# Kernel tuning notes

Measured on AMD Instinct MI355X. Metric: run time of the kernel, lower is better.

## Reference

```python
import jax, jax.numpy as jnp
import numpy as np


def setup_inputs() -> dict:
    key = jax.random.key(0)
    k1, k2 = jax.random.split(key)
    x = jax.random.normal(k1, (64, 64, 64, 64), dtype=jnp.float32)
    embeddings = jax.random.normal(k2, (400, 64), dtype=jnp.float32) * 0.1
    return {"x": x, "embeddings": embeddings}


def reference(x, embeddings):
    D = embeddings.shape[1]
    flat_x = x.reshape(-1, D)  # [N, D]
    # squared L2 distance via sum-of-squares + matmul: [N, K]
    distances = (
        jnp.sum(flat_x * flat_x, axis=1, keepdims=True)
        + jnp.sum(embeddings * embeddings, axis=1)
        - 2.0 * jnp.matmul(flat_x, embeddings.T)
    )
    encoding_indices = jnp.argmin(distances, axis=1)  # [N]
    quantized = jnp.take(embeddings, encoding_indices, axis=0)  # [N, D]
    return quantized.reshape(x.shape)
```

## Files before the change

### kernel.cpp

```cpp
#include <hip/hip_runtime.h>

#define D 64
#define K 400
#define KT 25
#define BLOCK 256
#define WPB (BLOCK / 64)
#define NRM_OFF 102400

typedef _Float16 f16x8 __attribute__((ext_vector_type(8)));
typedef float f32x4 __attribute__((ext_vector_type(4)));
typedef int i32x4 __attribute__((ext_vector_type(4)));


__global__ void vq_prep(const float* __restrict__ emb, void* __restrict__ ws) {
  _Float16* B = (_Float16*)ws;
  float* nrm = (float*)((char*)ws + NRM_OFF);
  int gid = blockIdx.x * blockDim.x + threadIdx.x;
  if (gid < KT * 4 * 64) {
    int t = gid >> 8;
    int f = (gid >> 6) & 3;
    int l = gid & 63;
    int code = t * 16 + (l & 15);
    int kb = ((l >> 4) << 3) + ((f >> 1) << 5);
    const float* ep = emb + code * D + kb;
    float4 u = *(const float4*)ep;
    float4 w = *(const float4*)(ep + 4);
    f16x8 h;
    if ((f & 1) == 0) {
      h[0] = (_Float16)(2.0f * u.x);
      h[1] = (_Float16)(2.0f * u.y);
      h[2] = (_Float16)(2.0f * u.z);
      h[3] = (_Float16)(2.0f * u.w);
      h[4] = (_Float16)(2.0f * w.x);
      h[5] = (_Float16)(2.0f * w.y);
      h[6] = (_Float16)(2.0f * w.z);
      h[7] = (_Float16)(2.0f * w.w);
    } else {
#define LOC(j, val)                                    \
      do {                                             \
        float s_ = 2.0f * (val);                       \
        _Float16 t_ = (_Float16)s_;                    \
        h[j] = (_Float16)((s_ - (float)t_) * 2048.0f); \
      } while (0)
      LOC(0, u.x); LOC(1, u.y); LOC(2, u.z); LOC(3, u.w);
      LOC(4, w.x); LOC(5, w.y); LOC(6, w.z); LOC(7, w.w);
#undef LOC
    }
    *(f16x8*)&B[gid * 8] = h;
  }
  if (gid < K) {
    const float4* ep = (const float4*)(emb + (size_t)gid * D);
    float4 s4 = {0.f, 0.f, 0.f, 0.f};
#pragma unroll
    for (int d = 0; d < 16; ++d) {
      float4 v = ep[d];
      s4.x = fmaf(v.x, v.x, s4.x);
      s4.y = fmaf(v.y, v.y, s4.y);
      s4.z = fmaf(v.z, v.z, s4.z);
      s4.w = fmaf(v.w, v.w, s4.w);
    }
    nrm[gid] = (s4.x + s4.y) + (s4.z + s4.w);
  }
}

#define SPL(hh, ll, j, val)                          \
  do {                                               \
    float v_ = (val);                                \
    _Float16 t_ = (_Float16)v_;                      \
    (hh)[j] = t_;                                    \
    (ll)[j] = (_Float16)((v_ - (float)t_) * 2048.0f);\
  } while (0)

__global__ __launch_bounds__(BLOCK) void vq_mfma(
    const float* __restrict__ x,
    const float* __restrict__ emb,
    const void* __restrict__ ws,
    float* __restrict__ out,
    int nrows) {
  const f16x8* B = (const f16x8*)ws;
  const float* nrm = (const float*)((const char*)ws + NRM_OFF);

  const int tid = threadIdx.x;
  const int lane = tid & 63;
  const int wid = tid >> 6;
  const int gw = blockIdx.x * WPB + wid;
  const int nw = gridDim.x * WPB;
  const int l15 = lane & 15;
  const int q = lane >> 4;

#define LOADX(a)                                                   \
  do {                                                             \
    const float* xp_ = x + (size_t)(row0 + (a)*16 + l15) * D + q * 8; \
    float4 u0_ = *(const float4*)xp_;                              \
    float4 u1_ = *(const float4*)(xp_ + 4);                        \
    float4 w0_ = *(const float4*)(xp_ + 32);                       \
    float4 w1_ = *(const float4*)(xp_ + 36);                       \
    SPL(xh##a##0, xl##a##0, 0, u0_.x);                             \
    SPL(xh##a##0, xl##a##0, 1, u0_.y);                             \
    SPL(xh##a##0, xl##a##0, 2, u0_.z);                             \
    SPL(xh##a##0, xl##a##0, 3, u0_.w);                             \
    SPL(xh##a##0, xl##a##0, 4, u1_.x);                             \
    SPL(xh##a##0, xl##a##0, 5, u1_.y);                             \
    SPL(xh##a##0, xl##a##0, 6, u1_.z);                             \
    SPL(xh##a##0, xl##a##0, 7, u1_.w);                             \
    SPL(xh##a##1, xl##a##1, 0, w0_.x);                             \
    SPL(xh##a##1, xl##a##1, 1, w0_.y);                             \
    SPL(xh##a##1, xl##a##1, 2, w0_.z);                             \
    SPL(xh##a##1, xl##a##1, 3, w0_.w);                             \
    SPL(xh##a##1, xl##a##1, 4, w1_.x);                             \
    SPL(xh##a##1, xl##a##1, 5, w1_.y);                             \
    SPL(xh##a##1, xl##a##1, 6, w1_.z);                             \
    SPL(xh##a##1, xl##a##1, 7, w1_.w);                             \
  } while (0)

#define PROCA(a)                                                              \
  do {                                                                        \
    f32x4 ah_ = {nn, nn, nn, nn};                                             \
    f32x4 al_ = {0.f, 0.f, 0.f, 0.f};                                         \
    ah_ = __builtin_amdgcn_mfma_f32_16x16x32_f16(xh##a##0, b0, ah_, 0, 0, 0); \
    ah_ = __builtin_amdgcn_mfma_f32_16x16x32_f16(xh##a##1, b2, ah_, 0, 0, 0); \
    al_ = __builtin_amdgcn_mfma_f32_16x16x32_f16(xh##a##0, b1, al_, 0, 0, 0); \
    al_ = __builtin_amdgcn_mfma_f32_16x16x32_f16(xl##a##0, b0, al_, 0, 0, 0); \
    al_ = __builtin_amdgcn_mfma_f32_16x16x32_f16(xh##a##1, b3, al_, 0, 0, 0); \
    al_ = __builtin_amdgcn_mfma_f32_16x16x32_f16(xl##a##1, b2, al_, 0, 0, 0); \
    _Pragma("unroll") for (int i_ = 0; i_ < 4; ++i_) {                        \
      float m_ = fmaf(al_[i_], 4.8828125e-4f, ah_[i_]);    \
      bool gt_ = m_ > bm##a[i_];                                              \
      bm##a[i_] = gt_ ? m_ : bm##a[i_];                                       \
      bt##a[i_] = gt_ ? t : bt##a[i_];                                        \
    }                                                                         \
  } while (0)

#define RSTA(a, mm)                                                        \
  _Pragma("unroll") for (int i_ = 0; i_ < 4; ++i_) {                       \
    float ov_ = __shfl_xor(bm##a[i_], (mm), 64);                           \
    int ok_ = __shfl_xor(bk##a[i_], (mm), 64);                             \
    bool tk_ = (ov_ > bm##a[i_]) || ((ov_ == bm##a[i_]) && (ok_ < bk##a[i_])); \
    bm##a[i_] = tk_ ? ov_ : bm##a[i_];                                     \
    bk##a[i_] = tk_ ? ok_ : bk##a[i_];                                     \
  }

#define WRA(a)                                                \
  do {                                                        \
    int j_ = (lane >> 2) & 3;                                 \
    int k01_ = (j_ & 1) ? bk##a[1] : bk##a[0];                \
    int k23_ = (j_ & 1) ? bk##a[3] : bk##a[2];                \
    int kk_ = (j_ & 2) ? k23_ : k01_;                         \
    int r_ = row0 + (a)*16 + (lane >> 2);                     \
    const f32x4* src_ = (const f32x4*)(emb + (size_t)kk_ * D);\
    f32x4* dst_ = (f32x4*)(out + (size_t)r_ * D);             \
    _Pragma("unroll") for (int s_ = 0; s_ < 4; ++s_) {        \
      int idx_ = (lane & 3) + (s_ << 2);                      \
      dst_[idx_] = src_[idx_];                                \
    }                                                         \
  } while (0)

  const int ngrp = nrows >> 6;
  for (int g = gw; g < ngrp; g += nw) {
    const int row0 = g << 6;

    f16x8 xh00, xh01, xl00, xl01;
    f16x8 xh10, xh11, xl10, xl11;
    f16x8 xh20, xh21, xl20, xl21;
    f16x8 xh30, xh31, xl30, xl31;
    LOADX(0);
    LOADX(1);
    LOADX(2);
    LOADX(3);

    f32x4 bm0, bm1, bm2, bm3;
    i32x4 bt0, bt1, bt2, bt3;
    bm0 = bm1 = bm2 = bm3 = (f32x4){-3.4e38f, -3.4e38f, -3.4e38f, -3.4e38f};
    bt0 = bt1 = bt2 = bt3 = (i32x4){0, 0, 0, 0};

    for (int t = 0; t < KT; ++t) {
      f16x8 b0 = B[(t * 4 + 0) * 64 + lane];
      f16x8 b1 = B[(t * 4 + 1) * 64 + lane];
      f16x8 b2 = B[(t * 4 + 2) * 64 + lane];
      f16x8 b3 = B[(t * 4 + 3) * 64 + lane];
      float nn = -nrm[t * 16 + l15];
      PROCA(0);
      PROCA(1);
      PROCA(2);
      PROCA(3);
    }

    i32x4 bk0 = bt0 * 16 + l15;
    i32x4 bk1 = bt1 * 16 + l15;
    i32x4 bk2 = bt2 * 16 + l15;
    i32x4 bk3 = bt3 * 16 + l15;
#pragma unroll
    for (int mm = 1; mm <= 8; mm <<= 1) {
      RSTA(0, mm)
      RSTA(1, mm)
      RSTA(2, mm)
      RSTA(3, mm)
    }

    WRA(0);
    WRA(1);
    WRA(2);
    WRA(3);
  }
#undef LOADX
#undef PROCA
#undef RSTA
#undef WRA
}

extern "C" void kernel_launch(void* const* d_in, const int* in_sizes, int n_in,
                              void* d_out, int out_size, void* d_ws, size_t ws_size,
                              hipStream_t stream) {
  const float* x = (const float*)d_in[0];
  const float* emb = (const float*)d_in[1];
  float* out = (float*)d_out;
  int nrows = in_sizes[0] / D;
  vq_prep<<<25, 256, 0, stream>>>(emb, d_ws);
  vq_mfma<<<1024, BLOCK, 0, stream>>>(x, emb, d_ws, out, nrows);
}
```

Baseline: 154.3 us.

## Stage codebook hi halves in LDS, split hi/lo buffers, shrink per-wave row tile

Reorganizes the codebook workspace into separate hi and lo fp16 buffers. Each 1024-thread block copies the hi part and the code norms into shared memory, while the lo part is still read from global memory. Each wave now processes 32 rows instead of 64, which cuts register pressure so occupancy can rise (launch bounds request 8 waves). The trade-off is that each B load is reused across fewer rows, there is a block-wide prologue copy and sync, and the grid shape changes.

```diff
diff --git a/kernel.cpp b/kernel.cpp
--- a/kernel.cpp
+++ b/kernel.cpp
@@ -3,8 +3,9 @@
 #define D 64
 #define K 400
 #define KT 25
-#define BLOCK 256
+#define BLOCK 1024
 #define WPB (BLOCK / 64)
+#define LO_OFF 51200
 #define NRM_OFF 102400
 
 typedef _Float16 f16x8 __attribute__((ext_vector_type(8)));
@@ -13,40 +14,32 @@
 
 
 __global__ void vq_prep(const float* __restrict__ emb, void* __restrict__ ws) {
-  _Float16* B = (_Float16*)ws;
+  _Float16* hi = (_Float16*)ws;
+  _Float16* lo = (_Float16*)((char*)ws + LO_OFF);
   float* nrm = (float*)((char*)ws + NRM_OFF);
   int gid = blockIdx.x * blockDim.x + threadIdx.x;
-  if (gid < KT * 4 * 64) {
-    int t = gid >> 8;
-    int f = (gid >> 6) & 3;
+  if (gid < KT * 2 * 64) {
+    int t = gid >> 7;
+    int c = (gid >> 6) & 1;
     int l = gid & 63;
     int code = t * 16 + (l & 15);
-    int kb = ((l >> 4) << 3) + ((f >> 1) << 5);
+    int kb = ((l >> 4) << 3) + (c << 5);
     const float* ep = emb + code * D + kb;
     float4 u = *(const float4*)ep;
     float4 w = *(const float4*)(ep + 4);
-    f16x8 h;
-    if ((f & 1) == 0) {
-      h[0] = (_Float16)(2.0f * u.x);
-      h[1] = (_Float16)(2.0f * u.y);
-      h[2] = (_Float16)(2.0f * u.z);
-      h[3] = (_Float16)(2.0f * u.w);
-      h[4] = (_Float16)(2.0f * w.x);
-      h[5] = (_Float16)(2.0f * w.y);
-      h[6] = (_Float16)(2.0f * w.z);
-      h[7] = (_Float16)(2.0f * w.w);
-    } else {
-#define LOC(j, val)                                    \
-      do {                                             \
-        float s_ = 2.0f * (val);                       \
-        _Float16 t_ = (_Float16)s_;                    \
-        h[j] = (_Float16)((s_ - (float)t_) * 2048.0f); \
-      } while (0)
-      LOC(0, u.x); LOC(1, u.y); LOC(2, u.z); LOC(3, u.w);
-      LOC(4, w.x); LOC(5, w.y); LOC(6, w.z); LOC(7, w.w);
-#undef LOC
-    }
-    *(f16x8*)&B[gid * 8] = h;
+    f16x8 h, g;
+#define HL(j, val)                                     \
+    do {                                               \
+      float s_ = 2.0f * (val);                         \
+      _Float16 t_ = (_Float16)s_;                      \
+      h[j] = t_;                                       \
+      g[j] = (_Float16)((s_ - (float)t_) * 2048.0f);   \
+    } while (0)
+    HL(0, u.x); HL(1, u.y); HL(2, u.z); HL(3, u.w);
+    HL(4, w.x); HL(5, w.y); HL(6, w.z); HL(7, w.w);
+#undef HL
+    *(f16x8*)&hi[gid * 8] = h;
+    *(f16x8*)&lo[gid * 8] = g;
   }
   if (gid < K) {
     const float4* ep = (const float4*)(emb + (size_t)gid * D);
@@ -71,16 +64,26 @@
     (ll)[j] = (_Float16)((v_ - (float)t_) * 2048.0f);\
   } while (0)
 
-__global__ __launch_bounds__(BLOCK) void vq_mfma(
+__global__ __launch_bounds__(BLOCK, 8) void vq_mfma(
     const float* __restrict__ x,
     const float* __restrict__ emb,
     const void* __restrict__ ws,
     float* __restrict__ out,
     int nrows) {
-  const f16x8* B = (const f16x8*)ws;
-  const float* nrm = (const float*)((const char*)ws + NRM_OFF);
+  __shared__ __align__(16) _Float16 sHi[KT][2][64][8];
+  __shared__ float sN[K];
+
+  const f16x8* gHi = (const f16x8*)ws;
+  const f16x8* gLo = (const f16x8*)((const char*)ws + LO_OFF);
+  const float* gN = (const float*)((const char*)ws + NRM_OFF);
 
   const int tid = threadIdx.x;
+
+  f16x8* sHiF = (f16x8*)&sHi[0][0][0][0];
+  for (int e = tid; e < KT * 2 * 64; e += BLOCK) sHiF[e] = gHi[e];
+  for (int k = tid; k < K; k += BLOCK) sN[k] = gN[k];
+  __syncthreads();
+
   const int lane = tid & 63;
   const int wid = tid >> 6;
   const int gw = blockIdx.x * WPB + wid;
@@ -113,22 +116,22 @@
     SPL(xh##a##1, xl##a##1, 7, w1_.w);                             \
   } while (0)
 
-#define PROCA(a)                                                              \
-  do {                                                                        \
-    f32x4 ah_ = {nn, nn, nn, nn};                                             \
-    f32x4 al_ = {0.f, 0.f, 0.f, 0.f};                                         \
-    ah_ = __builtin_amdgcn_mfma_f32_16x16x32_f16(xh##a##0, b0, ah_, 0, 0, 0); \
-    ah_ = __builtin_amdgcn_mfma_f32_16x16x32_f16(xh##a##1, b2, ah_, 0, 0, 0); \
-    al_ = __builtin_amdgcn_mfma_f32_16x16x32_f16(xh##a##0, b1, al_, 0, 0, 0); \
-    al_ = __builtin_amdgcn_mfma_f32_16x16x32_f16(xl##a##0, b0, al_, 0, 0, 0); \
-    al_ = __builtin_amdgcn_mfma_f32_16x16x32_f16(xh##a##1, b3, al_, 0, 0, 0); \
-    al_ = __builtin_amdgcn_mfma_f32_16x16x32_f16(xl##a##1, b2, al_, 0, 0, 0); \
-    _Pragma("unroll") for (int i_ = 0; i_ < 4; ++i_) {                        \
-      float m_ = fmaf(al_[i_], 4.8828125e-4f, ah_[i_]);    \
-      bool gt_ = m_ > bm##a[i_];                                              \
-      bm##a[i_] = gt_ ? m_ : bm##a[i_];                                       \
-      bt##a[i_] = gt_ ? t : bt##a[i_];                                        \
-    }                                                                         \
+#define PROCA(a)                                                               \
+  do {                                                                         \
+    f32x4 ah_ = {nn, nn, nn, nn};                                              \
+    f32x4 al_ = {0.f, 0.f, 0.f, 0.f};                                          \
+    ah_ = __builtin_amdgcn_mfma_f32_16x16x32_f16(xh##a##0, b0h, ah_, 0, 0, 0); \
+    ah_ = __builtin_amdgcn_mfma_f32_16x16x32_f16(xh##a##1, b1h, ah_, 0, 0, 0); \
+    al_ = __builtin_amdgcn_mfma_f32_16x16x32_f16(xl##a##0, b0h, al_, 0, 0, 0); \
+    al_ = __builtin_amdgcn_mfma_f32_16x16x32_f16(xl##a##1, b1h, al_, 0, 0, 0); \
+    al_ = __builtin_amdgcn_mfma_f32_16x16x32_f16(xh##a##0, b0l, al_, 0, 0, 0); \
+    al_ = __builtin_amdgcn_mfma_f32_16x16x32_f16(xh##a##1, b1l, al_, 0, 0, 0); \
+    _Pragma("unroll") for (int i_ = 0; i_ < 4; ++i_) {                         \
+      float m_ = fmaf(al_[i_], 4.8828125e-4f, ah_[i_]);     \
+      bool gt_ = m_ > bm##a[i_];                                               \
+      bm##a[i_] = gt_ ? m_ : bm##a[i_];                                        \
+      bt##a[i_] = gt_ ? t : bt##a[i_];                                         \
+    }                                                                          \
   } while (0)
 
 #define RSTA(a, mm)                                                        \
@@ -155,52 +158,40 @@
     }                                                         \
   } while (0)
 
-  const int ngrp = nrows >> 6;
-  for (int g = gw; g < ngrp; g += nw) {
-    const int row0 = g << 6;
+  const int npair = nrows >> 5;
+  for (int g = gw; g < npair; g += nw) {
+    const int row0 = g << 5;
 
     f16x8 xh00, xh01, xl00, xl01;
     f16x8 xh10, xh11, xl10, xl11;
-    f16x8 xh20, xh21, xl20, xl21;
-    f16x8 xh30, xh31, xl30, xl31;
     LOADX(0);
     LOADX(1);
-    LOADX(2);
-    LOADX(3);
-
-    f32x4 bm0, bm1, bm2, bm3;
-    i32x4 bt0, bt1, bt2, bt3;
-    bm0 = bm1 = bm2 = bm3 = (f32x4){-3.4e38f, -3.4e38f, -3.4e38f, -3.4e38f};
-    bt0 = bt1 = bt2 = bt3 = (i32x4){0, 0, 0, 0};
+
+    f32x4 bm0, bm1;
+    i32x4 bt0, bt1;
+    bm0 = bm1 = (f32x4){-3.4e38f, -3.4e38f, -3.4e38f, -3.4e38f};
+    bt0 = bt1 = (i32x4){0, 0, 0, 0};
 
     for (int t = 0; t < KT; ++t) {
-      f16x8 b0 = B[(t * 4 + 0) * 64 + lane];
-      f16x8 b1 = B[(t * 4 + 1) * 64 + lane];
-      f16x8 b2 = B[(t * 4 + 2) * 64 + lane];
-      f16x8 b3 = B[(t * 4 + 3) * 64 + lane];
-      float nn = -nrm[t * 16 + l15];
+      f16x8 b0h = *(const f16x8*)&sHi[t][0][lane][0];
+      f16x8 b1h = *(const f16x8*)&sHi[t][1][lane][0];
+      f16x8 b0l = gLo[(t * 2 + 0) * 64 + lane];
+      f16x8 b1l = gLo[(t * 2 + 1) * 64 + lane];
+      float nn = -sN[t * 16 + l15];
       PROCA(0);
       PROCA(1);
-      PROCA(2);
-      PROCA(3);
     }
 
     i32x4 bk0 = bt0 * 16 + l15;
     i32x4 bk1 = bt1 * 16 + l15;
-    i32x4 bk2 = bt2 * 16 + l15;
-    i32x4 bk3 = bt3 * 16 + l15;
 #pragma unroll
     for (int mm = 1; mm <= 8; mm <<= 1) {
       RSTA(0, mm)
       RSTA(1, mm)
-      RSTA(2, mm)
-      RSTA(3, mm)
     }
 
     WRA(0);
     WRA(1);
-    WRA(2);
-    WRA(3);
   }
 #undef LOADX
 #undef PROCA
@@ -215,6 +206,6 @@
   const float* emb = (const float*)d_in[1];
   float* out = (float*)d_out;
   int nrows = in_sizes[0] / D;
-  vq_prep<<<25, 256, 0, stream>>>(emb, d_ws);
-  vq_mfma<<<1024, BLOCK, 0, stream>>>(x, emb, d_ws, out, nrows);
+  vq_prep<<<13, 256, 0, stream>>>(emb, d_ws);
+  vq_mfma<<<512, BLOCK, 0, stream>>>(x, emb, d_ws, out, nrows);
 }
```

After: 289.3 us. 1.87x slower.
